# Kernel optimization log

Hardware: AMD Instinct MI355X
Metric: run time of the kernel (lower is better)

Reference implementation:

```python
import jax, jax.numpy as jnp
import numpy as np
from jax.scipy.special import digamma

# dims: B batch, N tokens, D ambient input dim, H heads, HD head ambient dim, DS spatial per head
B, N, D, H = 8, 1024, 512, 8
HD = D // H          # 64
DS = HD - 1          # 63
EPS = 1e-7
SCALE = 1.0 / np.sqrt(HD)
CURVATURE = -1.0     # k = -curvature = 1


def setup_inputs() -> dict:
    key = jax.random.key(0)
    ks = jax.random.split(key, 4)
    # points on the Lorentz hyperboloid: t = sqrt(||x_s||^2 + 1)
    x_s = jax.random.normal(ks[0], (B, N, D - 1), dtype=jnp.float32) * 0.5
    x_t = jnp.sqrt(jnp.sum(x_s * x_s, -1, keepdims=True) + 1.0)
    x = jnp.concatenate([x_t, x_s], -1)
    init = lambda k, sh: jax.random.normal(k, sh, dtype=jnp.float32) * (1.0 / np.sqrt(D))
    Wq = init(ks[1], (H, D, DS)); Wk = init(ks[2], (H, D, DS)); Wv = init(ks[3], (H, D, DS))
    bq = jnp.zeros((H, DS), jnp.float32); bk = jnp.zeros((H, DS), jnp.float32); bv = jnp.zeros((H, DS), jnp.float32)
    return {"x": x, "Wq": Wq, "bq": bq, "Wk": Wk, "bk": bk, "Wv": Wv, "bv": bv}


def lorentz_fc(x, W, b):
    # LorentzFC per head, vectorized over heads: spatial z = Wx+b, time from constraint
    z = jnp.einsum('bnd,hde->bhne', x, W) + b[None, :, None, :]   # [B,H,N,DS]
    t = jnp.sqrt(jnp.sum(z * z, -1, keepdims=True) + 1.0)
    return jnp.concatenate([t, z], -1)                            # [B,H,N,HD]


def lorentz_inner(q, k):
    time = jnp.einsum('bhni,bhmi->bhnm', q[..., :1], k[..., :1])
    space = jnp.einsum('bhnd,bhmd->bhnm', q[..., 1:], k[..., 1:])
    return -time + space


def logmap0(v):
    t, vs = v[..., :1], v[..., 1:]
    d = jnp.arccosh(jnp.maximum(t, 1.0 + EPS))
    denom = jnp.sqrt(jnp.maximum(t * t - 1.0, EPS))
    us = (d / denom) * vs
    return jnp.concatenate([jnp.zeros_like(t), us], -1)


def expmap0(u):
    us = u[..., 1:]
    r = jnp.sqrt(jnp.maximum(jnp.sum(us * us, -1, keepdims=True), EPS * EPS))
    t = jnp.cosh(r)
    xs = (jnp.sinh(r) / r) * us
    return jnp.concatenate([t, xs], -1)


def reference(x, Wq, bq, Wk, bk, Wv, bv):
    q = lorentz_fc(x, Wq, bq)
    k = lorentz_fc(x, Wk, bk)
    v = lorentz_fc(x, Wv, bv)
    scores = lorentz_inner(q, k) * SCALE            # [B,H,N,N]
    attn = jax.nn.softmax(scores, axis=-1)
    v_tan = logmap0(v)                              # [B,H,N,HD], time comp = 0
    out_tan = jnp.einsum('bhnm,bhmd->bhnd', attn, v_tan)
    out = expmap0(out_tan)                          # [B,H,N,HD]
    # curvature-aware log-radius head concat
    s = jnp.exp(0.5 * (digamma(jnp.asarray(H * DS / 2.0)) - digamma(jnp.asarray(DS / 2.0))))
    invK = 1.0 / CURVATURE                          # -1
    t_h = out[..., 0]                               # [B,H,N]
    u_h = out[..., 1:]                              # [B,H,N,DS]
    u_tilde = s * u_h
    sum_term = jnp.sum(t_h * t_h + invK, axis=1)    # [B,N]
    t_prime = jnp.sqrt(jnp.maximum(s * s * sum_term - invK, 1e-8))
    u_concat = jnp.transpose(u_tilde, (0, 2, 1, 3)).reshape(B, N, H * DS)
    return jnp.concatenate([t_prime[..., None], u_concat], -1)   # [B,N,1+H*DS]
```

## Files before the change

### kernel.cpp

```cpp
#include <hip/hip_runtime.h>
#include <math.h>

#define B_ 8
#define N_ 1024
#define D_ 512
#define H_ 8
#define HD_ 64
#define DS_ 63
#define SCALE_ 0.125f
#define EPS_ 1e-7f
#define KT_ 64

typedef short bf16x8 __attribute__((ext_vector_type(8)));
typedef float f32x16 __attribute__((ext_vector_type(16)));

typedef const __attribute__((address_space(1))) unsigned int* gas_ptr;
typedef __attribute__((address_space(3))) unsigned int* las_ptr;

__device__ inline ushort f2bf(float f) {
    uint u = __float_as_uint(f);
    uint r = (u + 0x7FFFu + ((u >> 16) & 1u)) >> 16;
    return (ushort)r;
}

__global__ void prep_kernel(const float* __restrict__ x,
                            const float* __restrict__ Wq, const float* __restrict__ Wk,
                            const float* __restrict__ Wv,
                            ushort* __restrict__ xb, ushort* __restrict__ Wt) {
    __shared__ float til[64 * 65];
    const int bid = blockIdx.x;
    if (bid < 4096) {
        int i = bid * 256 + threadIdx.x;
        float4 v = ((const float4*)x)[i];
        ushort4 o;
        o.x = f2bf(v.x); o.y = f2bf(v.y); o.z = f2bf(v.z); o.w = f2bf(v.w);
        ((ushort4*)xb)[i] = o;
    } else {
        const int b2 = bid - 4096;
        const int g = b2 >> 3, kbase = (b2 & 7) * 64;
        const int mat = g >> 3, h = g & 7;
        const float* W = (mat == 0) ? Wq : (mat == 1) ? Wk : Wv;
        const float* src = W + (size_t)h * D_ * DS_ + (size_t)kbase * DS_;
        for (int i = threadIdx.x; i < 64 * DS_; i += 256) {
            int k = i / DS_, e = i - k * DS_;
            til[k * 65 + e] = src[i];
        }
        __syncthreads();
        for (int i = threadIdx.x; i < 64 * 64; i += 256) {
            int e = i >> 6, kk = i & 63;
            float v = (e < DS_) ? til[kk * 65 + e] : 0.f;
            Wt[((size_t)g * 64 + e) * D_ + kbase + kk] = f2bf(v);
        }
    }
}

__global__ __launch_bounds__(256, 2)
void proj3_kernel(const ushort* __restrict__ Xb, const ushort* __restrict__ Wt,
                  const float* __restrict__ bq, const float* __restrict__ bk,
                  const float* __restrict__ bv,
                  ushort* __restrict__ Qo, ushort* __restrict__ Ko,
                  ushort* __restrict__ Vto)
{
    __shared__ char smem[65536];

    const int tid = threadIdx.x;
    const int wid = tid >> 6, lane = tid & 63;
    const int lm = lane & 31, g = lane >> 5;
    const int wr = wid & 1, wg = wid >> 1;
    const int R0 = blockIdx.x * 128;
    const int grp0 = blockIdx.y * 2;
    const int mat = grp0 >> 3;

    char* As = smem;
    char* Bs = smem + 32768;
    const ushort* Wg = Wt + (size_t)grp0 * 64 * D_;

    f32x16 acc00 = {0.f}, acc01 = {0.f}, acc10 = {0.f}, acc11 = {0.f};

    auto stageA = [&](int buf, int ktE) {
#pragma unroll
        for (int it = 0; it < 4; it++) {
            int ci = it * 256 + tid;
            int row = ci >> 3, cb = (ci & 7) * 16;
            const char* src = (const char*)(Xb + (size_t)(R0 + row) * D_ + ktE)
                              + (cb ^ ((row & 7) << 4));
            __builtin_amdgcn_global_load_lds((gas_ptr)src,
                (las_ptr)(As + buf * 16384 + it * 4096 + wid * 1024), 16, 0, 0);
        }
    };
    auto stageB = [&](int buf, int ktE) {
#pragma unroll
        for (int it = 0; it < 4; it++) {
            int ci = it * 256 + tid;
            int row = ci >> 3, cb = (ci & 7) * 16;
            const char* src = (const char*)(Wg + (size_t)row * D_ + ktE)
                              + (cb ^ ((row & 7) << 4));
            __builtin_amdgcn_global_load_lds((gas_ptr)src,
                (las_ptr)(Bs + buf * 16384 + it * 4096 + wid * 1024), 16, 0, 0);
        }
    };

    stageA(0, 0); stageB(0, 0);
    const int asw = (lm & 7) << 4;

    for (int t = 0; t < 8; t++) {
        __syncthreads();
        if (t < 7) { stageA((t + 1) & 1, (t + 1) * KT_); stageB((t + 1) & 1, (t + 1) * KT_); }
        const int cur = t & 1;
        char* Ab = As + cur * 16384;
        char* Bb = Bs + cur * 16384;
#pragma unroll
        for (int c = 0; c < 4; c++) {
            int kb = (c * 32 + g * 16) ^ asw;
            bf16x8 a0 = *(const bf16x8*)(Ab + (wr * 64 + lm) * 128 + kb);
            bf16x8 a1 = *(const bf16x8*)(Ab + (wr * 64 + 32 + lm) * 128 + kb);
            bf16x8 b0 = *(const bf16x8*)(Bb + (wg * 64 + lm) * 128 + kb);
            bf16x8 b1 = *(const bf16x8*)(Bb + (wg * 64 + 32 + lm) * 128 + kb);
            acc00 = __builtin_amdgcn_mfma_f32_32x32x16_bf16(a0, b0, acc00, 0, 0, 0);
            acc01 = __builtin_amdgcn_mfma_f32_32x32x16_bf16(a0, b1, acc01, 0, 0, 0);
            acc10 = __builtin_amdgcn_mfma_f32_32x32x16_bf16(a1, b0, acc10, 0, 0, 0);
            acc11 = __builtin_amdgcn_mfma_f32_32x32x16_bf16(a1, b1, acc11, 0, 0, 0);
        }
    }
    __syncthreads();

    float* zs   = (float*)smem;
    float* tval = (float*)(smem + 33280);
    float* cval = tval + 128;
    const float* bptr = (mat == 0) ? bq : (mat == 1) ? bk : bv;
    const int b = R0 >> 10, n0 = R0 & (N_ - 1);

    for (int pass = 0; pass < 2; pass++) {
        const int h = (grp0 + pass) & 7;
        if (pass) __syncthreads();
        if (wg == pass) {
            float ba = (lm < DS_) ? bptr[h * DS_ + lm] : 0.f;
            float bb = (lm + 32 < DS_) ? bptr[h * DS_ + lm + 32] : 0.f;
#pragma unroll
            for (int r = 0; r < 16; r++) {
                int rm = (r & 3) + 8 * (r >> 2) + 4 * g;
                zs[(wr * 64 + rm) * 65 + lm]           = acc00[r] + ba;
                zs[(wr * 64 + rm) * 65 + 32 + lm]      = acc01[r] + bb;
                zs[(wr * 64 + 32 + rm) * 65 + lm]      = acc10[r] + ba;
                zs[(wr * 64 + 32 + rm) * 65 + 32 + lm] = acc11[r] + bb;
            }
        }
        __syncthreads();
        if (tid < 128) {
            float ss = 0.f;
            for (int e = 0; e < DS_; e++) { float v = zs[tid * 65 + e]; ss += v * v; }
            float t = sqrtf(ss + 1.f);
            float w0, coef;
            if (mat == 0)      { w0 = -t * SCALE_; coef = SCALE_; }
            else if (mat == 1) { w0 =  t;          coef = 1.f; }
            else {
                float tc = fmaxf(t, 1.f + EPS_);
                float d  = acoshf(tc);
                float dn = sqrtf(fmaxf(t * t - 1.f, EPS_));
                w0 = 0.f; coef = d / dn;
            }
            tval[tid] = w0; cval[tid] = coef;
        }
        __syncthreads();

        const int bh = b * H_ + h;
        if (mat == 2) {
            for (int i = tid; i < 128 * 64; i += 256) {
                int e = i >> 7, nl = i & 127;
                float val = (e == 0) ? 0.f : cval[nl] * zs[nl * 65 + e - 1];
                Vto[((size_t)bh * 64 + e) * N_ + n0 + nl] = f2bf(val);
            }
        } else {
            ushort* dst = (mat == 0) ? Qo : Ko;
            for (int i = tid; i < 128 * 64; i += 256) {
                int rr = i >> 6, e = i & 63;
                float val = (e == 0) ? tval[rr] : cval[rr] * zs[rr * 65 + e - 1];
                dst[((size_t)bh * N_ + n0 + rr) * 64 + e] = f2bf(val);
            }
        }
    }
}

__global__ __launch_bounds__(128, 2)
void attn4_kernel(const ushort* __restrict__ Q, const ushort* __restrict__ K,
                  const ushort* __restrict__ Vt, float* __restrict__ out,
                  float* __restrict__ TS, float sconst)
{
    __shared__ char lds[32768];

    const int tid  = threadIdx.x;
    const int wid  = tid >> 6;
    const int lane = tid & 63;
    const int lm = lane & 31, g = lane >> 5;

    const int bid = blockIdx.x;
    const int bh  = (bid >> 7) * 8 + (bid & 7);
    const int R0  = ((bid >> 3) & 15) * 64;
    const int qrow = R0 + wid * 32 + lm;

    bf16x8 qf[4];
    const ushort* qptr = Q + (((size_t)bh) * N_ + qrow) * 64 + g * 8;
#pragma unroll
    for (int c = 0; c < 4; c++)
        qf[c] = *(const bf16x8*)(qptr + c * 16);

    f32x16 acc0 = {0.f}, acc1 = {0.f};
    float den = 0.f;

    const ushort* kg = K  + ((size_t)bh) * N_ * 64;
    const ushort* vg = Vt + ((size_t)bh) * 64 * N_;

    auto stage = [&](int buf, int kt) {
#pragma unroll
        for (int it = 0; it < 4; it++) {
            int ci = it * 128 + tid;
            int row = ci >> 3, cb = (ci & 7) << 4;
            int sw = (row & 7) << 4;
            const char* srck = (const char*)(kg + (size_t)(kt + row) * 64) + (cb ^ sw);
            __builtin_amdgcn_global_load_lds((gas_ptr)srck,
                (las_ptr)(lds + buf * 8192 + it * 2048 + wid * 1024), 16, 0, 0);
            const char* srcv = (const char*)(vg + (size_t)row * N_ + kt) + (cb ^ sw);
            __builtin_amdgcn_global_load_lds((gas_ptr)srcv,
                (las_ptr)(lds + 16384 + buf * 8192 + it * 2048 + wid * 1024), 16, 0, 0);
        }
    };

    stage(0, 0);
    for (int t = 0; t < 16; t++) {
        __syncthreads();
        if (t < 15) stage((t + 1) & 1, (t + 1) * KT_);
        const int cur = t & 1;
        char* kbase = lds + cur * 8192;
        char* vbase = lds + 16384 + cur * 8192;

#pragma unroll
        for (int sub = 0; sub < 2; sub++) {
            f32x16 st = {0.f};
            const int krow = sub * 32 + lm;
            const int ksw  = (krow & 7) << 4;
            __builtin_amdgcn_s_setprio(1);
#pragma unroll
            for (int c = 0; c < 4; c++) {
                bf16x8 kf = *(const bf16x8*)(kbase + krow * 128 + ((g * 16 + c * 32) ^ ksw));
                st = __builtin_amdgcn_mfma_f32_32x32x16_bf16(kf, qf[c], st, 0, 0, 0);
            }
            __builtin_amdgcn_s_setprio(0);
            float p[16];
#pragma unroll
            for (int rr = 0; rr < 16; rr++) {
                p[rr] = __expf(st[rr]);
                den += p[rr];
            }
            union { uint u[8]; bf16x8 v[2]; } pu;
#pragma unroll
            for (int j = 0; j < 8; j++)
                pu.u[j] = __builtin_amdgcn_perm(__float_as_uint(p[2 * j + 1]),
                                                __float_as_uint(p[2 * j]), 0x07060302);
            __builtin_amdgcn_s_setprio(1);
#pragma unroll
            for (int c = 0; c < 2; c++) {
#pragma unroll
                for (int dh = 0; dh < 2; dh++) {
                    const int vrow = dh * 32 + lm;
                    const int vsw  = (vrow & 7) << 4;
                    const int colb = sub * 64 + 8 * g + 32 * c;
                    union { uint2 u2[2]; bf16x8 v; } uu;
                    uu.u2[0] = *(const uint2*)(vbase + vrow * 128 + ( colb       ^ vsw));
                    uu.u2[1] = *(const uint2*)(vbase + vrow * 128 + ((colb + 16) ^ vsw));
                    if (dh == 0)
                        acc0 = __builtin_amdgcn_mfma_f32_32x32x16_bf16(uu.v, pu.v[c], acc0, 0, 0, 0);
                    else
                        acc1 = __builtin_amdgcn_mfma_f32_32x32x16_bf16(uu.v, pu.v[c], acc1, 0, 0, 0);
                }
            }
            __builtin_amdgcn_s_setprio(0);
        }
    }

    den += __shfl_xor(den, 32);
    float invd = 1.f / den;
    float ss = 0.f;
#pragma unroll
    for (int r = 0; r < 16; r++) {
        acc0[r] *= invd; acc1[r] *= invd;
        ss += acc0[r] * acc0[r] + acc1[r] * acc1[r];
    }
    ss += __shfl_xor(ss, 32);
    float rr = sqrtf(fmaxf(ss, 1e-14f));
    float t  = coshf(rr);
    float coef = sconst * sinhf(rr) / rr;

    const int b = bh >> 3, h = bh & 7;
    const size_t ob = ((size_t)b * N_ + qrow) * 505 + (size_t)h * DS_;
#pragma unroll
    for (int r = 0; r < 16; r++) {
        int d = (r & 3) + 8 * (r >> 2) + 4 * g;
        if (d >= 1) out[ob + d] = coef * acc0[r];
        out[ob + d + 32] = coef * acc1[r];
    }
    if (g == 0) TS[((size_t)bh) * N_ + qrow] = t;
}

__global__ void tprime_kernel(const float* __restrict__ TS, float* __restrict__ out,
                              float sconst)
{
    int idx = blockIdx.x * 256 + threadIdx.x;
    if (idx >= B_ * N_) return;
    int b = idx >> 10, n = idx & (N_ - 1);
    float sum = 0.f;
#pragma unroll
    for (int h = 0; h < H_; h++) {
        float t = TS[((size_t)(b * H_ + h)) * N_ + n];
        sum += t * t - 1.f;
    }
    float tp = sqrtf(fmaxf(sconst * sconst * sum + 1.f, 1e-8f));
    out[(size_t)idx * 505] = tp;
}

static double digamma_(double x) {
    double r = 0.0;
    while (x < 20.0) { r -= 1.0 / x; x += 1.0; }
    double f = 1.0 / (x * x);
    return r + log(x) - 0.5 / x - f * (1.0 / 12.0 - f * (1.0 / 120.0 - f * (1.0 / 252.0)));
}

extern "C" void kernel_launch(void* const* d_in, const int* in_sizes, int n_in,
                              void* d_out, int out_size, void* d_ws, size_t ws_size,
                              hipStream_t stream) {
    const float* x  = (const float*)d_in[0];
    const float* Wq = (const float*)d_in[1];
    const float* bq = (const float*)d_in[2];
    const float* Wk = (const float*)d_in[3];
    const float* bk = (const float*)d_in[4];
    const float* Wv = (const float*)d_in[5];
    const float* bv = (const float*)d_in[6];
    float* out = (float*)d_out;

    const size_t QKV = (size_t)B_ * H_ * N_ * 64;
    ushort* Qd  = (ushort*)d_ws;
    ushort* Kd  = Qd + QKV;
    ushort* Vtd = Kd + QKV;
    ushort* Xb  = Vtd + QKV;
    ushort* Wtd = Xb + (size_t)B_ * N_ * D_;
    float*  TS  = (float*)(Wtd + (size_t)24 * 64 * D_);

    const float sconst = (float)exp(0.5 * (digamma_(H_ * DS_ / 2.0) - digamma_(DS_ / 2.0)));

    prep_kernel<<<4096 + 192, 256, 0, stream>>>(x, Wq, Wk, Wv, Xb, Wtd);
    proj3_kernel<<<dim3(64, 12), 256, 0, stream>>>(Xb, Wtd, bq, bk, bv, Qd, Kd, Vtd);
    attn4_kernel<<<1024, 128, 0, stream>>>(Qd, Kd, Vtd, out, TS, sconst);
    tprime_kernel<<<(B_ * N_ + 255) / 256, 256, 0, stream>>>(TS, out, sconst);
}
```

Baseline: 83.68 us.

## Split attention key range across two wave pairs and fold softmax denominator into V

The attention kernel now uses 256 threads per block. Two wave-pair groups each process half of the key sequence and their partial accumulators are reduced through LDS at the end. The V time component is set to 1 so the softmax denominator comes out of the PV MFMA, which removes the per-element sum. Double buffering is dropped in favour of a load, sync, compute pattern per tile, which exposes load latency but doubles the waves working on each query tile.

```diff
diff --git a/kernel.cpp b/kernel.cpp
--- a/kernel.cpp
+++ b/kernel.cpp
@@ -167,7 +167,7 @@
         if (mat == 2) {
             for (int i = tid; i < 128 * 64; i += 256) {
                 int e = i >> 7, nl = i & 127;
-                float val = (e == 0) ? 0.f : cval[nl] * zs[nl * 65 + e - 1];
+                float val = (e == 0) ? 1.0f : cval[nl] * zs[nl * 65 + e - 1];
                 Vto[((size_t)bh * 64 + e) * N_ + n0 + nl] = f2bf(val);
             }
         } else {
@@ -181,22 +181,24 @@
     }
 }
 
-__global__ __launch_bounds__(128, 2)
-void attn4_kernel(const ushort* __restrict__ Q, const ushort* __restrict__ K,
+__global__ __launch_bounds__(256, 4)
+void attn5_kernel(const ushort* __restrict__ Q, const ushort* __restrict__ K,
                   const ushort* __restrict__ Vt, float* __restrict__ out,
                   float* __restrict__ TS, float sconst)
 {
     __shared__ char lds[32768];
 
     const int tid  = threadIdx.x;
-    const int wid  = tid >> 6;
     const int lane = tid & 63;
     const int lm = lane & 31, g = lane >> 5;
+    const int r = (tid >> 6) & 1, s = tid >> 7;
+    const int ptid = tid & 127, pw = ptid >> 6;
 
     const int bid = blockIdx.x;
-    const int bh  = (bid >> 7) * 8 + (bid & 7);
-    const int R0  = ((bid >> 3) & 15) * 64;
-    const int qrow = R0 + wid * 32 + lm;
+    const int idx = bid >> 3;
+    const int bh  = (idx >> 4) * 8 + (bid & 7);
+    const int R0  = (idx & 15) * 64;
+    const int qrow = R0 + r * 32 + lm;
 
     bf16x8 qf[4];
     const ushort* qptr = Q + (((size_t)bh) * N_ + qrow) * 64 + g * 8;
@@ -205,33 +207,28 @@
         qf[c] = *(const bf16x8*)(qptr + c * 16);
 
     f32x16 acc0 = {0.f}, acc1 = {0.f};
-    float den = 0.f;
 
     const ushort* kg = K  + ((size_t)bh) * N_ * 64;
     const ushort* vg = Vt + ((size_t)bh) * 64 * N_;
-
-    auto stage = [&](int buf, int kt) {
+    char* kbase = lds + s * 8192;
+    char* vbase = lds + 16384 + s * 8192;
+
+    for (int t = 0; t < 8; t++) {
+        __syncthreads();
+        const int ks = s * 512 + t * 64;
 #pragma unroll
         for (int it = 0; it < 4; it++) {
-            int ci = it * 128 + tid;
+            int ci = it * 128 + ptid;
             int row = ci >> 3, cb = (ci & 7) << 4;
             int sw = (row & 7) << 4;
-            const char* srck = (const char*)(kg + (size_t)(kt + row) * 64) + (cb ^ sw);
+            const char* srck = (const char*)(kg + (size_t)(ks + row) * 64) + (cb ^ sw);
             __builtin_amdgcn_global_load_lds((gas_ptr)srck,
-                (las_ptr)(lds + buf * 8192 + it * 2048 + wid * 1024), 16, 0, 0);
-            const char* srcv = (const char*)(vg + (size_t)row * N_ + kt) + (cb ^ sw);
+                (las_ptr)(kbase + it * 2048 + pw * 1024), 16, 0, 0);
+            const char* srcv = (const char*)(vg + (size_t)row * N_ + ks) + (cb ^ sw);
             __builtin_amdgcn_global_load_lds((gas_ptr)srcv,
-                (las_ptr)(lds + 16384 + buf * 8192 + it * 2048 + wid * 1024), 16, 0, 0);
-        }
-    };
-
-    stage(0, 0);
-    for (int t = 0; t < 16; t++) {
-        __syncthreads();
-        if (t < 15) stage((t + 1) & 1, (t + 1) * KT_);
-        const int cur = t & 1;
-        char* kbase = lds + cur * 8192;
-        char* vbase = lds + 16384 + cur * 8192;
+                (las_ptr)(vbase + it * 2048 + pw * 1024), 16, 0, 0);
+        }
+        __syncthreads();
 
 #pragma unroll
         for (int sub = 0; sub < 2; sub++) {
@@ -247,10 +244,8 @@
             __builtin_amdgcn_s_setprio(0);
             float p[16];
 #pragma unroll
-            for (int rr = 0; rr < 16; rr++) {
+            for (int rr = 0; rr < 16; rr++)
                 p[rr] = __expf(st[rr]);
-                den += p[rr];
-            }
             union { uint u[8]; bf16x8 v[2]; } pu;
 #pragma unroll
             for (int j = 0; j < 8; j++)
@@ -277,28 +272,45 @@
         }
     }
 
-    den += __shfl_xor(den, 32);
-    float invd = 1.f / den;
-    float ss = 0.f;
-#pragma unroll
-    for (int r = 0; r < 16; r++) {
-        acc0[r] *= invd; acc1[r] *= invd;
-        ss += acc0[r] * acc0[r] + acc1[r] * acc1[r];
-    }
-    ss += __shfl_xor(ss, 32);
-    float rr = sqrtf(fmaxf(ss, 1e-14f));
-    float t  = coshf(rr);
-    float coef = sconst * sinhf(rr) / rr;
-
-    const int b = bh >> 3, h = bh & 7;
-    const size_t ob = ((size_t)b * N_ + qrow) * 505 + (size_t)h * DS_;
-#pragma unroll
-    for (int r = 0; r < 16; r++) {
-        int d = (r & 3) + 8 * (r >> 2) + 4 * g;
-        if (d >= 1) out[ob + d] = coef * acc0[r];
-        out[ob + d + 32] = coef * acc1[r];
-    }
-    if (g == 0) TS[((size_t)bh) * N_ + qrow] = t;
+    __syncthreads();
+    float* fl = (float*)lds;
+    const int ib = (((r * 2 + g) * 32) + lm) * 32;
+    if (s == 1) {
+#pragma unroll
+        for (int j = 0; j < 16; j++) { fl[ib + j] = acc0[j]; fl[ib + 16 + j] = acc1[j]; }
+    }
+    __syncthreads();
+    if (s == 0) {
+#pragma unroll
+        for (int j = 0; j < 16; j++) { acc0[j] += fl[ib + j]; acc1[j] += fl[ib + 16 + j]; }
+
+        float draw = acc0[0];
+        float doth = __shfl_xor(draw, 32);
+        float den  = (g == 0) ? draw : doth;
+        if (g == 0) acc0[0] = 0.f;
+
+        float invd = 1.f / den;
+        float ss = 0.f;
+#pragma unroll
+        for (int j = 0; j < 16; j++) {
+            acc0[j] *= invd; acc1[j] *= invd;
+            ss += acc0[j] * acc0[j] + acc1[j] * acc1[j];
+        }
+        ss += __shfl_xor(ss, 32);
+        float rr = sqrtf(fmaxf(ss, 1e-14f));
+        float t  = coshf(rr);
+        float coef = sconst * sinhf(rr) / rr;
+
+        const int b = bh >> 3, h = bh & 7;
+        const size_t ob = ((size_t)b * N_ + qrow) * 505 + (size_t)h * DS_;
+#pragma unroll
+        for (int j = 0; j < 16; j++) {
+            int d = (j & 3) + 8 * (j >> 2) + 4 * g;
+            if (d >= 1) out[ob + d] = coef * acc0[j];
+            out[ob + d + 32] = coef * acc1[j];
+        }
+        if (g == 0) TS[((size_t)bh) * N_ + qrow] = t;
+    }
 }
 
 __global__ void tprime_kernel(const float* __restrict__ TS, float* __restrict__ out,
@@ -348,6 +360,6 @@
 
     prep_kernel<<<4096 + 192, 256, 0, stream>>>(x, Wq, Wk, Wv, Xb, Wtd);
     proj3_kernel<<<dim3(64, 12), 256, 0, stream>>>(Xb, Wtd, bq, bk, bv, Qd, Kd, Vtd);
-    attn4_kernel<<<1024, 128, 0, stream>>>(Qd, Kd, Vtd, out, TS, sconst);
+    attn5_kernel<<<1024, 256, 0, stream>>>(Qd, Kd, Vtd, out, TS, sconst);
     tprime_kernel<<<(B_ * N_ + 255) / 256, 256, 0, stream>>>(TS, out, sconst);
 }
```

Result: faster. 79.20 us (-5.4%).

## Widen attention blocks to eight waves and fold softmax denominator into PV MFMA

Applied to the files above, without the earlier changes.

The attention kernel now runs 512-thread blocks covering 256 query rows, so each staged K/V tile is shared by eight waves instead of two and there are four times fewer blocks. Each thread issues one async load per tile instead of four. The unused time column of V (previously zero) is set to 1.0, so the P·V MFMA also accumulates the softmax row sum and the per-element denominator additions disappear. The trade-offs are a denominator summed from bf16-rounded probabilities and 256 blocks, which may fill the GPU less evenly.

```diff
diff --git a/kernel.cpp b/kernel.cpp
--- a/kernel.cpp
+++ b/kernel.cpp
@@ -167,7 +167,7 @@
         if (mat == 2) {
             for (int i = tid; i < 128 * 64; i += 256) {
                 int e = i >> 7, nl = i & 127;
-                float val = (e == 0) ? 0.f : cval[nl] * zs[nl * 65 + e - 1];
+                float val = (e == 0) ? 1.0f : cval[nl] * zs[nl * 65 + e - 1];
                 Vto[((size_t)bh * 64 + e) * N_ + n0 + nl] = f2bf(val);
             }
         } else {
@@ -181,8 +181,8 @@
     }
 }
 
-__global__ __launch_bounds__(128, 2)
-void attn4_kernel(const ushort* __restrict__ Q, const ushort* __restrict__ K,
+__global__ __launch_bounds__(512, 2)
+void attn6_kernel(const ushort* __restrict__ Q, const ushort* __restrict__ K,
                   const ushort* __restrict__ Vt, float* __restrict__ out,
                   float* __restrict__ TS, float sconst)
 {
@@ -194,8 +194,8 @@
     const int lm = lane & 31, g = lane >> 5;
 
     const int bid = blockIdx.x;
-    const int bh  = (bid >> 7) * 8 + (bid & 7);
-    const int R0  = ((bid >> 3) & 15) * 64;
+    const int bh  = (bid >> 5) * 8 + (bid & 7);
+    const int R0  = ((bid >> 3) & 3) * 256;
     const int qrow = R0 + wid * 32 + lm;
 
     bf16x8 qf[4];
@@ -205,24 +205,19 @@
         qf[c] = *(const bf16x8*)(qptr + c * 16);
 
     f32x16 acc0 = {0.f}, acc1 = {0.f};
-    float den = 0.f;
 
     const ushort* kg = K  + ((size_t)bh) * N_ * 64;
     const ushort* vg = Vt + ((size_t)bh) * 64 * N_;
 
     auto stage = [&](int buf, int kt) {
-#pragma unroll
-        for (int it = 0; it < 4; it++) {
-            int ci = it * 128 + tid;
-            int row = ci >> 3, cb = (ci & 7) << 4;
-            int sw = (row & 7) << 4;
-            const char* srck = (const char*)(kg + (size_t)(kt + row) * 64) + (cb ^ sw);
-            __builtin_amdgcn_global_load_lds((gas_ptr)srck,
-                (las_ptr)(lds + buf * 8192 + it * 2048 + wid * 1024), 16, 0, 0);
-            const char* srcv = (const char*)(vg + (size_t)row * N_ + kt) + (cb ^ sw);
-            __builtin_amdgcn_global_load_lds((gas_ptr)srcv,
-                (las_ptr)(lds + 16384 + buf * 8192 + it * 2048 + wid * 1024), 16, 0, 0);
-        }
+        int row = tid >> 3, cb = (tid & 7) << 4;
+        int sw = (row & 7) << 4;
+        const char* srck = (const char*)(kg + (size_t)(kt + row) * 64) + (cb ^ sw);
+        __builtin_amdgcn_global_load_lds((gas_ptr)srck,
+            (las_ptr)(lds + buf * 8192 + wid * 1024), 16, 0, 0);
+        const char* srcv = (const char*)(vg + (size_t)row * N_ + kt) + (cb ^ sw);
+        __builtin_amdgcn_global_load_lds((gas_ptr)srcv,
+            (las_ptr)(lds + 16384 + buf * 8192 + wid * 1024), 16, 0, 0);
     };
 
     stage(0, 0);
@@ -247,10 +242,8 @@
             __builtin_amdgcn_s_setprio(0);
             float p[16];
 #pragma unroll
-            for (int rr = 0; rr < 16; rr++) {
+            for (int rr = 0; rr < 16; rr++)
                 p[rr] = __expf(st[rr]);
-                den += p[rr];
-            }
             union { uint u[8]; bf16x8 v[2]; } pu;
 #pragma unroll
             for (int j = 0; j < 8; j++)
@@ -277,13 +270,17 @@
         }
     }
 
-    den += __shfl_xor(den, 32);
+    float draw = acc0[0];
+    float doth = __shfl_xor(draw, 32);
+    float den  = (g == 0) ? draw : doth;
+    if (g == 0) acc0[0] = 0.f;
+
     float invd = 1.f / den;
     float ss = 0.f;
 #pragma unroll
-    for (int r = 0; r < 16; r++) {
-        acc0[r] *= invd; acc1[r] *= invd;
-        ss += acc0[r] * acc0[r] + acc1[r] * acc1[r];
+    for (int j = 0; j < 16; j++) {
+        acc0[j] *= invd; acc1[j] *= invd;
+        ss += acc0[j] * acc0[j] + acc1[j] * acc1[j];
     }
     ss += __shfl_xor(ss, 32);
     float rr = sqrtf(fmaxf(ss, 1e-14f));
@@ -293,10 +290,10 @@
     const int b = bh >> 3, h = bh & 7;
     const size_t ob = ((size_t)b * N_ + qrow) * 505 + (size_t)h * DS_;
 #pragma unroll
-    for (int r = 0; r < 16; r++) {
-        int d = (r & 3) + 8 * (r >> 2) + 4 * g;
-        if (d >= 1) out[ob + d] = coef * acc0[r];
-        out[ob + d + 32] = coef * acc1[r];
+    for (int j = 0; j < 16; j++) {
+        int d = (j & 3) + 8 * (j >> 2) + 4 * g;
+        if (d >= 1) out[ob + d] = coef * acc0[j];
+        out[ob + d + 32] = coef * acc1[j];
     }
     if (g == 0) TS[((size_t)bh) * N_ + qrow] = t;
 }
@@ -348,6 +345,6 @@
 
     prep_kernel<<<4096 + 192, 256, 0, stream>>>(x, Wq, Wk, Wv, Xb, Wtd);
     proj3_kernel<<<dim3(64, 12), 256, 0, stream>>>(Xb, Wtd, bq, bk, bv, Qd, Kd, Vtd);
-    attn4_kernel<<<1024, 128, 0, stream>>>(Qd, Kd, Vtd, out, TS, sconst);
+    attn6_kernel<<<256, 512, 0, stream>>>(Qd, Kd, Vtd, out, TS, sconst);
     tprime_kernel<<<(B_ * N_ + 255) / 256, 256, 0, stream>>>(TS, out, sconst);
 }
```

After: 78.09 us. -6.7%, faster.
